# Kernel optimization log

Hardware: AMD Instinct MI355X
Metric: run time of the kernel (lower is better)

Reference implementation:

```python
import jax, jax.numpy as jnp
import numpy as np

N = 50000
E = 800000
IN_DIM = 3
HID = 128
OUT_DIM = 3
RED = 16


def setup_inputs() -> dict:
    key = jax.random.key(0)
    ks = jax.random.split(key, 20)
    s = lambda k, shp: jax.random.normal(k, shp, dtype=jnp.float32) * 0.05
    inp = {
        'x': jax.random.normal(ks[0], (N, IN_DIM), dtype=jnp.float32),
        'edge_index': jax.random.randint(ks[1], (2, E), 0, N, dtype=jnp.int32),
        'deg_inv_sqrt': jax.random.uniform(ks[2], (N,), dtype=jnp.float32),
        # GCN layer weights (torch Linear convention: [out, in])
        'W1': s(ks[3], (HID, IN_DIM)), 'b1': s(ks[4], (HID,)),
        'W2': s(ks[5], (HID, HID)),    'b2': s(ks[6], (HID,)),
        'W3': s(ks[7], (HID, HID)),    'b3': s(ks[8], (HID,)),
        # channel attention MLPs (no bias): C -> C//RED -> C
        'ca1_w1': s(ks[9],  (HID // RED, HID)), 'ca1_w2': s(ks[10], (HID, HID // RED)),
        'ca2_w1': s(ks[11], (HID // RED, HID)), 'ca2_w2': s(ks[12], (HID, HID // RED)),
        'ca3_w1': s(ks[13], (HID // RED, HID)), 'ca3_w2': s(ks[14], (HID, HID // RED)),
        # output head
        'Wout': s(ks[15], (OUT_DIM, HID)), 'bout': s(ks[16], (OUT_DIM,)),
    }
    return inp


def _gcn(x, row, col, dis, W, b):
    # gather source features, normalize by deg_inv_sqrt[row]*deg_inv_sqrt[col], scatter-add to target
    norm = (dis[row] * dis[col])[:, None]          # [E,1]
    msg = x[row] * norm                             # [E,C]
    agg = jax.ops.segment_sum(msg, col, num_segments=x.shape[0])  # [N,C]
    return jax.nn.elu(agg @ W.T + b)


def _channel_attn(x, w1, w2):
    # global avg/max pool over nodes -> [C]; shared MLP; sigmoid gate
    avg = jnp.mean(x, axis=0)
    mx = jnp.max(x, axis=0)
    mlp = lambda v: jax.nn.relu(v @ w1.T) @ w2.T
    att = jax.nn.sigmoid(mlp(avg) + mlp(mx))        # [C]
    return x * att


def reference(x, edge_index, deg_inv_sqrt, W1, b1, W2, b2, W3, b3,
              ca1_w1, ca1_w2, ca2_w1, ca2_w2, ca3_w1, ca3_w2, Wout, bout):
    row, col = edge_index[0], edge_index[1]
    h = _gcn(x, row, col, deg_inv_sqrt, W1, b1)
    h = _channel_attn(h, ca1_w1, ca1_w2)
    h = _gcn(h, row, col, deg_inv_sqrt, W2, b2)
    h = _channel_attn(h, ca2_w1, ca2_w2)
    h = _gcn(h, row, col, deg_inv_sqrt, W3, b3)
    h = _channel_attn(h, ca3_w1, ca3_w2)
    return h @ Wout.T + bout
```

## Files before the change

kernel.cpp:

```cpp
#include <hip/hip_runtime.h>

#define NN 50000
#define NE 800000
#define NPAD 50176
#define NBD3 391
#define NBG 782
#define PMAX (NBG*128)
#define NRED 64

#define EC 4096
#define NBLKC 196
#define NBUCK 1563
#define LT (NBUCK*NBLKC)
#define NS1 300
#define DCAP 1024

typedef __attribute__((ext_vector_type(8))) short bf16x8;
typedef __attribute__((ext_vector_type(4))) float f32x4;

__device__ __forceinline__ float elu_f(float x){ return x > 0.f ? x : __expf(x) - 1.f; }

__device__ __forceinline__ ushort f2bf(float f){
    unsigned u = __float_as_uint(f);
    unsigned r = (u + 0x7FFFu + ((u >> 16) & 1u)) >> 16;
    return (ushort)r;
}
__device__ __forceinline__ float bf2f(short u){
    return __uint_as_float(((unsigned)(unsigned short)u) << 16);
}

__global__ __launch_bounds__(256) void k_bhist(const int* __restrict__ col, int* __restrict__ hist){
    __shared__ int h[NBUCK];
    int blk = blockIdx.x;
    for (int i = threadIdx.x; i < NBUCK; i += 256) h[i] = 0;
    __syncthreads();
    int base = blk * EC;
    #pragma unroll
    for (int i = 0; i < 16; ++i){
        int e = base + i*256 + threadIdx.x;
        if (e < NE) atomicAdd(&h[col[e] >> 5], 1);
    }
    __syncthreads();
    for (int i = threadIdx.x; i < NBUCK; i += 256) hist[i*NBLKC + blk] = h[i];
}

__global__ __launch_bounds__(256) void k_s1(const int* __restrict__ hist, int* __restrict__ bsum){
    __shared__ int red[256];
    int base = blockIdx.x*1024 + threadIdx.x;
    int s = 0;
    #pragma unroll
    for (int i = 0; i < 4; ++i){ int idx = base + i*256; if (idx < LT) s += hist[idx]; }
    red[threadIdx.x] = s;
    __syncthreads();
    for (int off = 128; off > 0; off >>= 1){
        if (threadIdx.x < off) red[threadIdx.x] += red[threadIdx.x + off];
        __syncthreads();
    }
    if (threadIdx.x == 0) bsum[blockIdx.x] = red[0];
}

__global__ __launch_bounds__(512) void k_s2(const int* __restrict__ bsum, int* __restrict__ boff){
    __shared__ int s[512];
    int t = threadIdx.x;
    int v = (t < NS1) ? bsum[t] : 0;
    s[t] = v;
    __syncthreads();
    for (int off = 1; off < 512; off <<= 1){
        int u = (t >= off) ? s[t - off] : 0;
        __syncthreads();
        s[t] += u;
        __syncthreads();
    }
    if (t < NS1) boff[t] = s[t] - v;
}

__global__ __launch_bounds__(256) void k_s3(const int* __restrict__ hist, const int* __restrict__ boff,
                                            int* __restrict__ scanned, int* __restrict__ bucketPtr){
    __shared__ int red[256];
    int blk = blockIdx.x, t = threadIdx.x;
    int base = blk*1024;
    int v[4]; int s = 0;
    #pragma unroll
    for (int i = 0; i < 4; ++i){
        int idx = base + t*4 + i;
        v[i] = (idx < LT) ? hist[idx] : 0;
        s += v[i];
    }
    red[t] = s;
    __syncthreads();
    for (int off = 1; off < 256; off <<= 1){
        int u = (t >= off) ? red[t - off] : 0;
        __syncthreads();
        red[t] += u;
        __syncthreads();
    }
    int run = boff[blk] + red[t] - s;
    #pragma unroll
    for (int i = 0; i < 4; ++i){
        int idx = base + t*4 + i;
        if (idx < LT){
            scanned[idx] = run;
            if (idx % NBLKC == 0) bucketPtr[idx / NBLKC] = run;
            run += v[i];
        }
    }
    if (blk == 0 && t == 0) bucketPtr[NBUCK] = NE;
}

__global__ __launch_bounds__(256) void k_csort(const int* __restrict__ row, const int* __restrict__ col,
                                               const int* __restrict__ scanned, int2* __restrict__ edgeS){
    __shared__ int curs[NBUCK];
    int blk = blockIdx.x;
    for (int i = threadIdx.x; i < NBUCK; i += 256) curs[i] = scanned[i*NBLKC + blk];
    __syncthreads();
    int base = blk * EC;
    #pragma unroll
    for (int i = 0; i < 16; ++i){
        int e = base + i*256 + threadIdx.x;
        if (e < NE){
            int r = row[e], c = col[e];
            int pos = atomicAdd(&curs[c >> 5], 1);
            edgeS[pos] = make_int2(r, c);
        }
    }
}

__global__ __launch_bounds__(256) void k_dsort(const float* __restrict__ dis, const int* __restrict__ bucketPtr,
                                               int2* __restrict__ edge, int* __restrict__ rowptr){
    __shared__ int nodeCnt[32];
    __shared__ int nodeOff[33];
    __shared__ float disL[32];
    __shared__ int2 stage[DCAP];
    int b = blockIdx.x, t = threadIdx.x;
    int j0 = bucketPtr[b], j1 = bucketPtr[b+1], cnt = j1 - j0;
    if (t < 32){
        nodeCnt[t] = 0;
        int c = b*32 + t;
        disL[t] = (c < NN) ? dis[c] : 0.f;
    }
    __syncthreads();
    int er[8], ec[8], rk[8]; int m = 0;
    for (int j = t; j < cnt && m < 8; j += 256){
        int2 e = edge[j0 + j];
        int cl = e.y & 31;
        er[m] = e.x; ec[m] = e.y;
        rk[m] = atomicAdd(&nodeCnt[cl], 1);
        ++m;
    }
    __syncthreads();
    if (t == 0){
        int run = 0;
        #pragma unroll
        for (int i = 0; i < 32; ++i){ nodeOff[i] = run; run += nodeCnt[i]; }
        nodeOff[32] = run;
    }
    __syncthreads();
    if (t < 32){
        int c = b*32 + t;
        if (c < NN) rowptr[c] = j0 + nodeOff[t];
    }
    if (b == 0 && t == 0) rowptr[NN] = NE;
    bool staged = (cnt <= DCAP);
    for (int i = 0; i < m; ++i){
        int r = er[i], cl = ec[i] & 31;
        float nm = dis[r] * disL[cl];
        int pos = nodeOff[cl] + rk[i];
        int2 rec = make_int2(r, __float_as_int(nm));
        if (staged) stage[pos] = rec;
        else        edge[j0 + pos] = rec;
    }
    __syncthreads();
    if (staged)
        for (int j = t; j < cnt; j += 256) edge[j0 + j] = stage[j];
}

__global__ __launch_bounds__(128) void k_l1(const float* __restrict__ x, const int* __restrict__ rowptr,
                        const int2* __restrict__ edge, const float* __restrict__ W,
                        const float* __restrict__ b, ushort* __restrict__ h, float* __restrict__ part){
    __shared__ float aggL[128*3];
    int t = threadIdx.x;
    int n0 = blockIdx.x * 128;
    int nEnd = min(n0 + 128, NN);
    {
        int n = n0 + t;
        float a0 = 0.f, a1 = 0.f, a2 = 0.f;
        if (n < NN){
            int j0 = rowptr[n], j1 = rowptr[n + 1];
            for (int j = j0; j < j1; ++j){
                int2 e = edge[j];
                int r = e.x; float w = __int_as_float(e.y);
                a0 = fmaf(x[r*3+0], w, a0);
                a1 = fmaf(x[r*3+1], w, a1);
                a2 = fmaf(x[r*3+2], w, a2);
            }
        }
        aggL[t*3+0] = a0; aggL[t*3+1] = a1; aggL[t*3+2] = a2;
    }
    __syncthreads();
    int c = t;
    float w0 = W[c*3+0], w1 = W[c*3+1], w2 = W[c*3+2], bb = b[c];
    float s = 0.f, m = -3.4e38f;
    for (int n = n0; n < nEnd; ++n){
        int nn = n - n0;
        float v = fmaf(aggL[nn*3+0], w0, fmaf(aggL[nn*3+1], w1, fmaf(aggL[nn*3+2], w2, bb)));
        v = elu_f(v);
        h[(size_t)n*128 + c] = f2bf(v);
        s += v; m = fmaxf(m, v);
    }
    part[blockIdx.x*128 + c] = s;
    part[PMAX + blockIdx.x*128 + c] = m;
}

__global__ __launch_bounds__(256) void k_gather128(const ushort* __restrict__ h,
                              const int* __restrict__ rowptr, const int2* __restrict__ edge,
                              ushort* __restrict__ aggB){
    int t = blockIdx.x * blockDim.x + threadIdx.x;
    int n = t >> 4, l = t & 15;
    if (n >= NN) return;
    int j0 = rowptr[n], j1 = rowptr[n + 1];
    float acc[8] = {0.f,0.f,0.f,0.f,0.f,0.f,0.f,0.f};
    int j = j0;
    for (; j + 3 < j1; j += 4){
        int2 e0 = edge[j], e1 = edge[j+1], e2 = edge[j+2], e3 = edge[j+3];
        bf16x8 v0 = *(const bf16x8*)(h + (size_t)e0.x*128 + l*8);
        bf16x8 v1 = *(const bf16x8*)(h + (size_t)e1.x*128 + l*8);
        bf16x8 v2 = *(const bf16x8*)(h + (size_t)e2.x*128 + l*8);
        bf16x8 v3 = *(const bf16x8*)(h + (size_t)e3.x*128 + l*8);
        float w0 = __int_as_float(e0.y), w1 = __int_as_float(e1.y);
        float w2 = __int_as_float(e2.y), w3 = __int_as_float(e3.y);
        #pragma unroll
        for (int c = 0; c < 8; ++c){
            acc[c] = fmaf(bf2f(v0[c]), w0, acc[c]);
            acc[c] = fmaf(bf2f(v1[c]), w1, acc[c]);
            acc[c] = fmaf(bf2f(v2[c]), w2, acc[c]);
            acc[c] = fmaf(bf2f(v3[c]), w3, acc[c]);
        }
    }
    for (; j < j1; ++j){
        int2 e0 = edge[j];
        bf16x8 v0 = *(const bf16x8*)(h + (size_t)e0.x*128 + l*8);
        float w0 = __int_as_float(e0.y);
        #pragma unroll
        for (int c = 0; c < 8; ++c)
            acc[c] = fmaf(bf2f(v0[c]), w0, acc[c]);
    }
    bf16x8 o;
    #pragma unroll
    for (int c = 0; c < 8; ++c)
        o[c] = (short)f2bf(acc[c]);
    *(bf16x8*)(aggB + (size_t)n*128 + l*8) = o;
}

__global__ __launch_bounds__(256) void k_attn_pre(const float* __restrict__ part, int nblk,
                                                  float* __restrict__ part2){
    __shared__ float sS[2][128], sM[2][128];
    int c = threadIdx.x & 127, g = threadIdx.x >> 7;
    float s = 0.f, m = -3.4e38f;
    for (int b = blockIdx.x*2 + g; b < nblk; b += NRED*2){
        s += part[b*128 + c];
        m = fmaxf(m, part[PMAX + b*128 + c]);
    }
    sS[g][c] = s; sM[g][c] = m;
    __syncthreads();
    if (g == 0){
        part2[blockIdx.x*128 + c] = sS[0][c] + sS[1][c];
        part2[NRED*128 + blockIdx.x*128 + c] = fmaxf(sM[0][c], sM[1][c]);
    }
}

__global__ __launch_bounds__(512) void k_attn(const float* __restrict__ part2,
                       const float* __restrict__ w1, const float* __restrict__ w2,
                       const float* __restrict__ Wsrc, void* __restrict__ Wdst, int mode){
    __shared__ float sAll[4][128], mAll[4][128];
    __shared__ float avg[128], mx[128], ha[8], hm[8], attL[128];
    int c = threadIdx.x & 127, g = threadIdx.x >> 7;
    float s = 0.f, m = -3.4e38f;
    #pragma unroll
    for (int b = 0; b < NRED/4; ++b){
        int r = b*4 + g;
        s += part2[r*128 + c];
        m = fmaxf(m, part2[NRED*128 + r*128 + c]);
    }
    sAll[g][c] = s; mAll[g][c] = m;
    __syncthreads();
    if (g == 0){
        s = sAll[0][c] + sAll[1][c] + sAll[2][c] + sAll[3][c];
        m = fmaxf(fmaxf(mAll[0][c], mAll[1][c]), fmaxf(mAll[2][c], mAll[3][c]));
        avg[c] = s / (float)NN;
        mx[c] = m;
    }
    __syncthreads();
    if (threadIdx.x < 8){
        int cc = threadIdx.x;
        float sa = 0.f, sm = 0.f;
        for (int k = 0; k < 128; ++k){
            float w = w1[cc*128 + k];
            sa += avg[k]*w; sm += mx[k]*w;
        }
        ha[cc] = fmaxf(sa, 0.f); hm[cc] = fmaxf(sm, 0.f);
    }
    __syncthreads();
    if (threadIdx.x < 128){
        float oa = 0.f, om = 0.f;
        for (int j = 0; j < 8; ++j){
            float w = w2[c*8 + j];
            oa += ha[j]*w; om += hm[j]*w;
        }
        attL[c] = 1.f / (1.f + __expf(-(oa + om)));
    }
    __syncthreads();
    if (mode == 0){
        ushort* wd = (ushort*)Wdst;
        for (int i = threadIdx.x; i < 16384; i += 512)
            wd[i] = f2bf(Wsrc[i] * attL[i & 127]);
    } else {
        float* wd = (float*)Wdst;
        if (threadIdx.x < 384)
            wd[threadIdx.x] = Wsrc[threadIdx.x] * attL[threadIdx.x & 127];
    }
}

__global__ __launch_bounds__(256) void k_gemm_mfma(const ushort* __restrict__ aggB,
                        const ushort* __restrict__ Wb, const float* __restrict__ b,
                        ushort* __restrict__ h, float* __restrict__ part){
    __shared__ float poolS[4][128], poolM[4][128];
    int tid = threadIdx.x;
    int wave = tid >> 6, l = tid & 63;
    int lr = l & 15, lk = l >> 4;
    int n0 = blockIdx.x * 64 + wave * 16;

    bf16x8 a[4];
    const ushort* arow = aggB + (size_t)(n0 + lr) * 128 + lk * 8;
    #pragma unroll
    for (int kb = 0; kb < 4; ++kb)
        a[kb] = *(const bf16x8*)(arow + kb * 32);

    float s_part[8], m_part[8];
    const ushort* wbase = Wb + (size_t)lr * 128 + lk * 8;
    #pragma unroll
    for (int t = 0; t < 8; ++t){
        int j0 = t * 16;
        float bias = b[j0 + lr];
        f32x4 acc = {bias, bias, bias, bias};
        const ushort* wrow = wbase + (size_t)j0 * 128;
        #pragma unroll
        for (int kb = 0; kb < 4; ++kb){
            bf16x8 bf = *(const bf16x8*)(wrow + kb * 32);
            acc = __builtin_amdgcn_mfma_f32_16x16x32_bf16(a[kb], bf, acc, 0, 0, 0);
        }
        float s = 0.f, m = -3.4e38f;
        #pragma unroll
        for (int r = 0; r < 4; ++r){
            int n = n0 + lk * 4 + r;
            float v = elu_f(acc[r]);
            if (n < NN){
                h[(size_t)n * 128 + j0 + lr] = f2bf(v);
                s += v; m = fmaxf(m, v);
            }
        }
        s += __shfl_xor(s, 16); s += __shfl_xor(s, 32);
        m = fmaxf(m, __shfl_xor(m, 16)); m = fmaxf(m, __shfl_xor(m, 32));
        s_part[t] = s; m_part[t] = m;
    }
    if (lk == 0){
        #pragma unroll
        for (int t = 0; t < 8; ++t){
            poolS[wave][t * 16 + lr] = s_part[t];
            poolM[wave][t * 16 + lr] = m_part[t];
        }
    }
    __syncthreads();
    if (tid < 128){
        float S = poolS[0][tid] + poolS[1][tid] + poolS[2][tid] + poolS[3][tid];
        float M = fmaxf(fmaxf(poolM[0][tid], poolM[1][tid]), fmaxf(poolM[2][tid], poolM[3][tid]));
        part[blockIdx.x * 128 + tid] = S;
        part[PMAX + blockIdx.x * 128 + tid] = M;
    }
}

__global__ __launch_bounds__(256) void k_out(const ushort* __restrict__ h,
                      const float* __restrict__ WoS, const float* __restrict__ bo,
                      float* __restrict__ out){
    int n = blockIdx.x * blockDim.x + threadIdx.x;
    if (n >= NN) return;
    float acc0 = bo[0], acc1 = bo[1], acc2 = bo[2];
    const bf16x8* hv = (const bf16x8*)(h + (size_t)n*128);
    #pragma unroll
    for (int i = 0; i < 16; ++i){
        bf16x8 v = hv[i];
        #pragma unroll
        for (int c = 0; c < 8; ++c){
            int cc = i*8 + c;
            float hv_f = bf2f(v[c]);
            acc0 = fmaf(hv_f, WoS[cc],        acc0);
            acc1 = fmaf(hv_f, WoS[128 + cc],  acc1);
            acc2 = fmaf(hv_f, WoS[256 + cc],  acc2);
        }
    }
    out[n*3+0] = acc0; out[n*3+1] = acc1; out[n*3+2] = acc2;
}

extern "C" void kernel_launch(void* const* d_in, const int* in_sizes, int n_in,
                              void* d_out, int out_size, void* d_ws, size_t ws_size,
                              hipStream_t stream) {
    const float* x    = (const float*)d_in[0];
    const int*   ei   = (const int*)d_in[1];
    const int*   row  = ei;
    const int*   col  = ei + NE;
    const float* dis  = (const float*)d_in[2];
    const float* W1   = (const float*)d_in[3];
    const float* b1   = (const float*)d_in[4];
    const float* W2   = (const float*)d_in[5];
    const float* b2   = (const float*)d_in[6];
    const float* W3   = (const float*)d_in[7];
    const float* b3   = (const float*)d_in[8];
    const float* ca1w1= (const float*)d_in[9];
    const float* ca1w2= (const float*)d_in[10];
    const float* ca2w1= (const float*)d_in[11];
    const float* ca2w2= (const float*)d_in[12];
    const float* ca3w1= (const float*)d_in[13];
    const float* ca3w2= (const float*)d_in[14];
    const float* Wout = (const float*)d_in[15];
    const float* bout = (const float*)d_in[16];
    float* out = (float*)d_out;

    ushort* hB    = (ushort*)d_ws;
    ushort* aggB  = hB + (size_t)NN*128;
    float*  part  = (float*)(aggB + (size_t)NPAD*128);
    float*  part2 = part + (size_t)2*PMAX;
    ushort* Wb2   = (ushort*)(part2 + 2*NRED*128);
    ushort* Wb3   = Wb2 + 16384;
    float*  WoutS = (float*)(Wb3 + 16384);
    int2*   edge  = (int2*)(WoutS + 384);
    int*    rowptr= (int*)(edge + NE);
    int*    hist  = rowptr + NN + 1;
    int*    scanned = hist + LT;
    int*    bucketPtr = scanned + LT;
    int*    bsum  = bucketPtr + NBUCK + 1;
    int*    boff  = bsum + NS1;

    const int gath_blocks = (NN * 16) / 256;

    k_bhist<<<NBLKC, 256, 0, stream>>>(col, hist);
    k_s1<<<NS1, 256, 0, stream>>>(hist, bsum);
    k_s2<<<1, 512, 0, stream>>>(bsum, boff);
    k_s3<<<NS1, 256, 0, stream>>>(hist, boff, scanned, bucketPtr);
    k_csort<<<NBLKC, 256, 0, stream>>>(row, col, scanned, edge);
    k_dsort<<<NBUCK, 256, 0, stream>>>(dis, bucketPtr, edge, rowptr);

    k_l1<<<NBD3, 128, 0, stream>>>(x, rowptr, edge, W1, b1, hB, part);
    k_attn_pre<<<NRED, 256, 0, stream>>>(part, NBD3, part2);
    k_attn<<<1, 512, 0, stream>>>(part2, ca1w1, ca1w2, W2, (void*)Wb2, 0);

    k_gather128<<<gath_blocks, 256, 0, stream>>>(hB, rowptr, edge, aggB);
    k_gemm_mfma<<<NBG, 256, 0, stream>>>(aggB, Wb2, b2, hB, part);
    k_attn_pre<<<NRED, 256, 0, stream>>>(part, NBG, part2);
    k_attn<<<1, 512, 0, stream>>>(part2, ca2w1, ca2w2, W3, (void*)Wb3, 0);

    k_gather128<<<gath_blocks, 256, 0, stream>>>(hB, rowptr, edge, aggB);
    k_gemm_mfma<<<NBG, 256, 0, stream>>>(aggB, Wb3, b3, hB, part);
    k_attn_pre<<<NRED, 256, 0, stream>>>(part, NBG, part2);
    k_attn<<<1, 512, 0, stream>>>(part2, ca3w1, ca3w2, Wout, (void*)WoutS, 1);

    k_out<<<(NN+255)/256, 256, 0, stream>>>(hB, WoutS, bout, out);
}
```

Measured before the change: 210.8 us.

## Sort nodes by degree to balance gather wavefront workloads

Adds a degree histogram, scan and permutation pass after the CSR build so that nodes are ordered by in-degree. The feature gather kernels then process nodes in this order, so the nodes sharing a wavefront have similar edge counts and the divergence from unequal loop lengths is reduced. The price is three extra small kernel launches plus a memset, and output rows are now written in a scattered node order.

```diff
diff --git a/kernel.cpp b/kernel.cpp
--- a/kernel.cpp
+++ b/kernel.cpp
@@ -7,6 +7,7 @@
 #define NBG 782
 #define PMAX (NBG*128)
 #define NRED 64
+#define NBN 196
 
 #define EC 4096
 #define NBLKC 196
@@ -172,6 +173,56 @@
     __syncthreads();
     if (staged)
         for (int j = t; j < cnt; j += 256) edge[j0 + j] = stage[j];
+}
+
+__global__ __launch_bounds__(256) void k_dhist(const int* __restrict__ rowptr, int* __restrict__ dh){
+    __shared__ int h[64];
+    int t = threadIdx.x;
+    if (t < 64) h[t] = 0;
+    __syncthreads();
+    int n = blockIdx.x*256 + t;
+    if (n < NN){
+        int deg = rowptr[n+1] - rowptr[n];
+        atomicAdd(&h[min(deg, 63)], 1);
+    }
+    __syncthreads();
+    if (t < 64 && h[t]) atomicAdd(&dh[t], h[t]);
+}
+
+__global__ __launch_bounds__(64) void k_dscan(const int* __restrict__ dh, int* __restrict__ dOff){
+    __shared__ int s[64];
+    int t = threadIdx.x;
+    int v = dh[t];
+    s[t] = v;
+    __syncthreads();
+    for (int off = 1; off < 64; off <<= 1){
+        int u = (t >= off) ? s[t - off] : 0;
+        __syncthreads();
+        s[t] += u;
+        __syncthreads();
+    }
+    dOff[t] = s[t] - v;
+}
+
+__global__ __launch_bounds__(256) void k_dperm(const int* __restrict__ rowptr, const int* __restrict__ dOff,
+                                               int* __restrict__ dcur, int* __restrict__ perm){
+    __shared__ int lcnt[64];
+    __shared__ int gbase[64];
+    int t = threadIdx.x;
+    if (t < 64) lcnt[t] = 0;
+    __syncthreads();
+    int n = blockIdx.x*256 + t;
+    int bin = 0, lrk = 0;
+    bool ok = (n < NN);
+    if (ok){
+        int deg = rowptr[n+1] - rowptr[n];
+        bin = min(deg, 63);
+        lrk = atomicAdd(&lcnt[bin], 1);
+    }
+    __syncthreads();
+    if (t < 64 && lcnt[t]) gbase[t] = atomicAdd(&dcur[t], lcnt[t]);
+    __syncthreads();
+    if (ok) perm[dOff[bin] + gbase[bin] + lrk] = n;
 }
 
 __global__ __launch_bounds__(128) void k_l1(const float* __restrict__ x, const int* __restrict__ rowptr,
@@ -213,10 +264,11 @@
 
 __global__ __launch_bounds__(256) void k_gather128(const ushort* __restrict__ h,
                               const int* __restrict__ rowptr, const int2* __restrict__ edge,
-                              ushort* __restrict__ aggB){
+                              const int* __restrict__ perm, ushort* __restrict__ aggB){
     int t = blockIdx.x * blockDim.x + threadIdx.x;
-    int n = t >> 4, l = t & 15;
-    if (n >= NN) return;
+    int tt = t >> 4, l = t & 15;
+    if (tt >= NN) return;
+    int n = perm[tt];
     int j0 = rowptr[n], j1 = rowptr[n + 1];
     float acc[8] = {0.f,0.f,0.f,0.f,0.f,0.f,0.f,0.f};
     int j = j0;
@@ -438,6 +490,10 @@
     int*    bucketPtr = scanned + LT;
     int*    bsum  = bucketPtr + NBUCK + 1;
     int*    boff  = bsum + NS1;
+    int*    dh    = boff + NS1;
+    int*    dcur  = dh + 64;
+    int*    dOff  = dcur + 64;
+    int*    perm  = dOff + 64;
 
     const int gath_blocks = (NN * 16) / 256;
 
@@ -446,18 +502,23 @@
     k_s2<<<1, 512, 0, stream>>>(bsum, boff);
     k_s3<<<NS1, 256, 0, stream>>>(hist, boff, scanned, bucketPtr);
     k_csort<<<NBLKC, 256, 0, stream>>>(row, col, scanned, edge);
+    hipMemsetAsync(dh, 0, 128*sizeof(int), stream);
     k_dsort<<<NBUCK, 256, 0, stream>>>(dis, bucketPtr, edge, rowptr);
+
+    k_dhist<<<NBN, 256, 0, stream>>>(rowptr, dh);
+    k_dscan<<<1, 64, 0, stream>>>(dh, dOff);
+    k_dperm<<<NBN, 256, 0, stream>>>(rowptr, dOff, dcur, perm);
 
     k_l1<<<NBD3, 128, 0, stream>>>(x, rowptr, edge, W1, b1, hB, part);
     k_attn_pre<<<NRED, 256, 0, stream>>>(part, NBD3, part2);
     k_attn<<<1, 512, 0, stream>>>(part2, ca1w1, ca1w2, W2, (void*)Wb2, 0);
 
-    k_gather128<<<gath_blocks, 256, 0, stream>>>(hB, rowptr, edge, aggB);
+    k_gather128<<<gath_blocks, 256, 0, stream>>>(hB, rowptr, edge, perm, aggB);
     k_gemm_mfma<<<NBG, 256, 0, stream>>>(aggB, Wb2, b2, hB, part);
     k_attn_pre<<<NRED, 256, 0, stream>>>(part, NBG, part2);
     k_attn<<<1, 512, 0, stream>>>(part2, ca2w1, ca2w2, W3, (void*)Wb3, 0);
 
-    k_gather128<<<gath_blocks, 256, 0, stream>>>(hB, rowptr, edge, aggB);
+    k_gather128<<<gath_blocks, 256, 0, stream>>>(hB, rowptr, edge, perm, aggB);
     k_gemm_mfma<<<NBG, 256, 0, stream>>>(aggB, Wb3, b3, hB, part);
     k_attn_pre<<<NRED, 256, 0, stream>>>(part, NBG, part2);
     k_attn<<<1, 512, 0, stream>>>(part2, ca3w1, ca3w2, Wout, (void*)WoutS, 1);
```

Result: slower. 228.0 us (+8.2%).
